# Optimization experiments

Measured on AMD Instinct MI355X. Metric: run time of the kernel, lower is better.

The kernel has to match this reference:

```python
import jax, jax.numpy as jnp
import numpy as np


def setup_inputs() -> dict:
    key = jax.random.key(0)
    ks = jax.random.split(key, 5)
    N, C, H, W = 4, 256, 64, 64
    fan_scale = 1.0 / np.sqrt(C)  # kaiming-ish scale for 1x1 conv weights
    x = jax.random.normal(ks[0], (N, C, H, W), dtype=jnp.float32)
    Wq = jax.random.normal(ks[1], (C, C), dtype=jnp.float32) * fan_scale
    Wk = jax.random.normal(ks[2], (C, C), dtype=jnp.float32) * fan_scale
    Wv = jax.random.normal(ks[3], (C, C), dtype=jnp.float32) * fan_scale
    bq = jnp.zeros((C,), dtype=jnp.float32)
    bk = jnp.zeros((C,), dtype=jnp.float32)
    bv = jnp.zeros((C,), dtype=jnp.float32)
    gamma = jax.random.uniform(ks[4], (1,), dtype=jnp.float32)
    return {"x": x, "Wq": Wq, "bq": bq, "Wk": Wk, "bk": bk, "Wv": Wv, "bv": bv, "gamma": gamma}


def reference(x, Wq, bq, Wk, bk, Wv, bv, gamma):
    # x: (N, C, H, W); 1x1 convs are channel-mixing matmuls.
    N, C, H, W = x.shape
    HW = H * W
    xf = x.reshape(N, C, HW)
    q = jnp.einsum('oc,ncl->nol', Wq, xf) + bq[None, :, None]  # (N, C, HW)
    k = jnp.einsum('oc,ncl->nol', Wk, xf) + bk[None, :, None]
    v = jnp.einsum('oc,ncl->nol', Wv, xf) + bv[None, :, None]
    # spatial mode: energy = softmax(Q^T K) over last dim (no 1/sqrt(d) scaling)
    energy = jax.nn.softmax(jnp.einsum('nci,ncj->nij', q, k), axis=-1)  # (N, HW, HW)
    # att[n,c,i] = sum_j v[n,c,j] * energy[n,i,j]  (bmm(value, energy^T))
    att = jnp.einsum('ncj,nij->nci', v, energy)  # (N, C, HW)
    # in_channels == out_channels -> residual is identity
    out = x + gamma[0] * att.reshape(N, C, H, W)
    return out
```

## Files before the change

### kernel.cpp

```cpp
#include <hip/hip_runtime.h>

typedef unsigned short ushort_t;
typedef unsigned int u32;
typedef _Float16 f16;
typedef f16 f16x8 __attribute__((ext_vector_type(8)));
typedef f16 f16x2 __attribute__((ext_vector_type(2)));
typedef ushort_t u16x8 __attribute__((ext_vector_type(8)));
typedef float f32x4 __attribute__((ext_vector_type(4)));
typedef float f32x16 __attribute__((ext_vector_type(16)));

#define C_DIM 256
#define HW 4096
#define CHW (C_DIM*HW)
#define L2E 1.4426950408889634f

__device__ __align__(16) f16 g_xbT[4 * CHW];
__device__ __align__(16) f16 g_q[4 * CHW];
__device__ __align__(16) f16 g_k[4 * CHW];
__device__ __align__(16) f16 g_v[4 * CHW];
__device__ __align__(16) f16 g_opart[16 * CHW];
__device__ __align__(16) float g_ml[16 * 2 * HW];
__device__ __align__(16) f16 g_wf[3 * 65536];
__device__ __align__(16) float g_bf[3 * 256];

__device__ __forceinline__ float bf2f(ushort_t h) {
    union { u32 u; float f; } v; v.u = ((u32)h) << 16; return v.f;
}
__device__ __forceinline__ ushort_t f2bf(float f) {
    union { float f; u32 u; } v; v.f = f;
    u32 r = v.u + 0x7FFF + ((v.u >> 16) & 1);
    return (ushort_t)(r >> 16);
}
__device__ __forceinline__ float fin0(float v) {
    return (v > -1e30f && v < 1e30f) ? v : 0.f;
}
__device__ __forceinline__ f16 sf16(float v) {
    return (f16)((v > -1e4f && v < 1e4f) ? v : 0.f);
}
__device__ __forceinline__ void gl2lds16(const f16* g, f16* l) {
    __builtin_amdgcn_global_load_lds(
        (const __attribute__((address_space(1))) u32*)g,
        (__attribute__((address_space(3))) u32*)l, 16, 0, 0);
}
__device__ __forceinline__ int probe_mode(const void* p) {
    int lane = threadIdx.x & 63;
    float v = fabsf(bf2f(((const ushort_t*)p)[lane]));
    v = (v < 1e6f) ? v : 1e6f;
#pragma unroll
    for (int d = 1; d < 64; d <<= 1) v += __shfl_xor(v, d, 64);
    return (v * (1.f / 64.f) > 100.f) ? 1 : 0;
}

__global__ void k_sentinel(ushort_t* out, int n) {
    int i = blockIdx.x * 256 + threadIdx.x;
    if (i < n) out[i] = f2bf(777.f);
}

__global__ __launch_bounds__(256) void k_wprep(
    const void* __restrict__ W0, const void* __restrict__ b0,
    const void* __restrict__ W1, const void* __restrict__ b1,
    const void* __restrict__ W2, const void* __restrict__ b2)
{
    int mat = blockIdx.y;
    const void* W = (mat == 0) ? W0 : (mat == 1) ? W1 : W2;
    const void* B = (mat == 0) ? b0 : (mat == 1) ? b1 : b2;
    int mode = probe_mode(W);
    int off = blockIdx.x * 2048 + threadIdx.x * 8;
    f16* dst = g_wf + mat * 65536 + off;
    f16x8 o;
    if (mode == 0) {
        u16x8 v = *(const u16x8*)((const ushort_t*)W + off);
#pragma unroll
        for (int e = 0; e < 8; ++e) o[e] = sf16(bf2f(v[e]));
    } else {
        const float* wf = (const float*)W + off;
        float4 a = *(const float4*)wf;
        float4 b = *(const float4*)(wf + 4);
        o[0]=sf16(a.x); o[1]=sf16(a.y); o[2]=sf16(a.z); o[3]=sf16(a.w);
        o[4]=sf16(b.x); o[5]=sf16(b.y); o[6]=sf16(b.z); o[7]=sf16(b.w);
    }
    *(f16x8*)dst = o;
    if (blockIdx.x == 0 && threadIdx.x < 32) {
#pragma unroll
        for (int e = 0; e < 8; ++e) {
            int i = threadIdx.x * 8 + e;
            g_bf[mat * 256 + i] = mode ? ((const float*)B)[i]
                                       : bf2f(((const ushort_t*)B)[i]);
        }
    }
}

__global__ __launch_bounds__(256) void k_transpose(const void* __restrict__ xv) {
    __shared__ f16 t[64][66];
    int mode = probe_mode(xv);
    int n = blockIdx.z, c0 = blockIdx.y * 64, l0 = blockIdx.x * 64;
    int tid = threadIdx.x;
    f16* ob = g_xbT + n * CHW;
    int lq = (tid & 15) * 4;
    int cl = tid >> 4;
    if (mode == 0) {
        const ushort_t* xb = (const ushort_t*)xv + n * CHW;
#pragma unroll
        for (int p = 0; p < 4; ++p) {
            int c = cl + 16 * p;
            ushort4 v = *(const ushort4*)(xb + (c0 + c) * HW + l0 + lq);
            t[lq + 0][c] = sf16(bf2f(v.x));
            t[lq + 1][c] = sf16(bf2f(v.y));
            t[lq + 2][c] = sf16(bf2f(v.z));
            t[lq + 3][c] = sf16(bf2f(v.w));
        }
    } else {
        const float* xb = (const float*)xv + n * CHW;
#pragma unroll
        for (int p = 0; p < 4; ++p) {
            int c = cl + 16 * p;
            float4 v = *(const float4*)(xb + (c0 + c) * HW + l0 + lq);
            t[lq + 0][c] = sf16(v.x);
            t[lq + 1][c] = sf16(v.y);
            t[lq + 2][c] = sf16(v.z);
            t[lq + 3][c] = sf16(v.w);
        }
    }
    __syncthreads();
    int c2 = (tid & 31) * 2;
    int lr = tid >> 5;
#pragma unroll
    for (int p = 0; p < 8; ++p) {
        int l = lr + 8 * p;
        u32 pair = *(const u32*)&t[l][c2];
        *(u32*)(ob + (l0 + l) * C_DIM + c0 + c2) = pair;
    }
}

__global__ __launch_bounds__(256) void k_proj() {
    __shared__ __align__(16) f16 lds_x[128 * 64];
    __shared__ __align__(16) f16 lds_w[128 * 64];
    int l0 = blockIdx.x * 128;
    int og0 = blockIdx.y * 128;
    int n = blockIdx.z;
    int mat = og0 >> 8;
    int om0 = og0 & 255;
    const f16* Wf = g_wf + mat * 65536;
    const float* Bf = g_bf + mat * 256;
    int tid = threadIdx.x, w = tid >> 6, lane = tid & 63;
    int quad = lane >> 4, l16 = lane & 15;
    const f16* xb = g_xbT + n * CHW;

    f32x4 acc[2][8];
#pragma unroll
    for (int a = 0; a < 2; a++)
#pragma unroll
        for (int b = 0; b < 8; b++) acc[a][b] = f32x4{0.f, 0.f, 0.f, 0.f};

    for (int ch = 0; ch < 4; ++ch) {
        int cc0 = ch * 64;
#pragma unroll
        for (int s = 0; s < 4; ++s) {
            int g = s * 256 + tid;
            int row = g >> 3, gp = (g & 7) ^ (row & 7);
            gl2lds16(xb + (l0 + row) * C_DIM + cc0 + gp * 8,
                     lds_x + (s * 256 + w * 64) * 8);
            gl2lds16(Wf + (om0 + row) * C_DIM + cc0 + gp * 8,
                     lds_w + (s * 256 + w * 64) * 8);
        }
        asm volatile("s_waitcnt vmcnt(0)" ::: "memory");
        __builtin_amdgcn_s_barrier();
        __builtin_amdgcn_sched_barrier(0);
#pragma unroll
        for (int ks = 0; ks < 2; ++ks) {
            f16x8 af[2];
#pragma unroll
            for (int mt = 0; mt < 2; ++mt) {
                int row = w * 32 + mt * 16 + l16;
                int g = ks * 4 + quad;
                int pos = g ^ (row & 7);
                af[mt] = *(const f16x8*)(lds_x + (row * 8 + pos) * 8);
            }
#pragma unroll
            for (int nt = 0; nt < 8; ++nt) {
                int rowo = nt * 16 + l16;
                int g = ks * 4 + quad;
                int pos = g ^ (rowo & 7);
                f16x8 bfv = *(const f16x8*)(lds_w + (rowo * 8 + pos) * 8);
                if (mat < 2) {
                    acc[0][nt] = __builtin_amdgcn_mfma_f32_16x16x32_f16(af[0], bfv, acc[0][nt], 0, 0, 0);
                    acc[1][nt] = __builtin_amdgcn_mfma_f32_16x16x32_f16(af[1], bfv, acc[1][nt], 0, 0, 0);
                } else {
                    acc[0][nt] = __builtin_amdgcn_mfma_f32_16x16x32_f16(bfv, af[0], acc[0][nt], 0, 0, 0);
                    acc[1][nt] = __builtin_amdgcn_mfma_f32_16x16x32_f16(bfv, af[1], acc[1][nt], 0, 0, 0);
                }
            }
        }
        __builtin_amdgcn_s_barrier();
    }

    if (mat < 2) {
        f16* T = ((mat == 0) ? g_q : g_k) + n * CHW;
        float bvv[8];
#pragma unroll
        for (int nt = 0; nt < 8; nt++) bvv[nt] = Bf[om0 + nt * 16 + l16];
#pragma unroll
        for (int mt = 0; mt < 2; mt++)
#pragma unroll
            for (int nt = 0; nt < 8; nt++)
#pragma unroll
                for (int r = 0; r < 4; r++) {
                    int l = l0 + w * 32 + mt * 16 + quad * 4 + r;
                    int o = om0 + nt * 16 + l16;
                    T[l * C_DIM + o] = sf16(acc[mt][nt][r] + bvv[nt]);
                }
    } else {
        f16* T = g_v + n * CHW;
#pragma unroll
        for (int mt = 0; mt < 2; mt++)
#pragma unroll
            for (int nt = 0; nt < 8; nt++)
#pragma unroll
                for (int r = 0; r < 4; r++) {
                    int o = om0 + nt * 16 + quad * 4 + r;
                    int l = l0 + w * 32 + mt * 16 + l16;
                    T[o * HW + l] = sf16(acc[mt][nt][r] + Bf[o]);
                }
    }
}

__device__ __forceinline__ f16x8 pack_pfrag(const float* p, int h) {
    union PK { u32 u; f16x2 h2; } t0, t1, t2, t3;
    t0.h2 = f16x2{(f16)p[0], (f16)p[1]};
    t1.h2 = f16x2{(f16)p[2], (f16)p[3]};
    t2.h2 = f16x2{(f16)p[4], (f16)p[5]};
    t3.h2 = f16x2{(f16)p[6], (f16)p[7]};
    u32 sa = __shfl_xor(t0.u, 32, 64);
    u32 sb = __shfl_xor(t1.u, 32, 64);
    u32 sc = __shfl_xor(t2.u, 32, 64);
    u32 sd = __shfl_xor(t3.u, 32, 64);
    union RW { u32 w[4]; f16x8 v; } r;
    r.w[0] = h ? sc : t0.u;
    r.w[1] = h ? sd : t1.u;
    r.w[2] = h ? t2.u : sa;
    r.w[3] = h ? t3.u : sb;
    return r.v;
}

__global__ __launch_bounds__(256, 2) void k_attn() {
    __shared__ __align__(16) f16 smem[32768];
    f16* kbuf = smem;
    f16* vbuf = smem + 16384;

    int bid = blockIdx.x;
    int x8 = bid & 7;
    int n = x8 >> 1, jhi = x8 & 1;
    int rest = bid >> 3;
    int jlo = rest & 1;
    int i0 = (rest >> 1) * 128;
    int jq = jhi * 2 + jlo;
    int tid = threadIdx.x, w = tid >> 6, lane = tid & 63;
    int j5 = lane & 31, h = lane >> 5;

    const f16* Qb = g_q + n * CHW;
    const f16* Kb = g_k + n * CHW;
    const f16* Vb = g_v + n * CHW;

    f16x8 qf[16];
    {
        const f16* qrow = Qb + (i0 + w * 32 + j5) * C_DIM + h * 8;
#pragma unroll
        for (int ck = 0; ck < 16; ++ck)
            qf[ck] = *(const f16x8*)(qrow + ck * 16);
    }

    int k_lane = h * 256 + j5 * 8;
    int v_lane = h * 2048 + j5 * 8;

    const f16* ksrc = Kb + (jq * 1024 + j5) * C_DIM + (w * 2 + h) * 8;
    const f16* vsrc = Vb + tid * HW + jq * 1024;
    int dst_w = w * 512;

    f32x16 o_acc[8];
#pragma unroll
    for (int ct = 0; ct < 8; ++ct)
#pragma unroll
        for (int r = 0; r < 16; ++r) o_acc[ct][r] = 0.f;

    float m_ = -1e30f, l_ = 0.f, al_prev = 1.f;
    f16x8 pf0 = {}, pf1 = {};

#pragma unroll
    for (int s = 0; s < 4; ++s) gl2lds16(ksrc + s * 64, kbuf + s * 2048 + dst_w);
    ksrc += 32 * C_DIM;
    asm volatile("s_waitcnt vmcnt(0)" ::: "memory");
    __builtin_amdgcn_s_barrier();
    __builtin_amdgcn_sched_barrier(0);

    for (int it = 0; it < 31; ++it) {
        int kcur = it & 1;
#pragma unroll
        for (int s = 0; s < 4; ++s)
            gl2lds16(ksrc + s * 64, kbuf + (kcur ^ 1) * 8192 + s * 2048 + dst_w);
        ksrc += 32 * C_DIM;
        __builtin_amdgcn_sched_barrier(0);
#pragma unroll
        for (int s = 0; s < 4; ++s)
            gl2lds16(vsrc + s * 8, vbuf + kcur * 8192 + s * 2048 + dst_w);
        vsrc += 32;
        __builtin_amdgcn_sched_barrier(0);

        const f16* kb = kbuf + kcur * 8192 + k_lane;
        f32x16 sa, sb;
#pragma unroll
        for (int r = 0; r < 16; ++r) { sa[r] = 0.f; sb[r] = 0.f; }
        __builtin_amdgcn_s_setprio(1);
#pragma unroll
        for (int ck = 0; ck < 16; ++ck) {
            f16x8 kf = *(const f16x8*)(kb + ck * 512);
            if (ck & 1) sb = __builtin_amdgcn_mfma_f32_32x32x16_f16(kf, qf[ck], sb, 0, 0, 0);
            else        sa = __builtin_amdgcn_mfma_f32_32x32x16_f16(kf, qf[ck], sa, 0, 0, 0);
        }
        __builtin_amdgcn_s_setprio(0);
        f32x16 st;
#pragma unroll
        for (int r = 0; r < 16; ++r) st[r] = sa[r] + sb[r];

        asm volatile("s_waitcnt vmcnt(8)" ::: "memory");
        __builtin_amdgcn_s_barrier();
        __builtin_amdgcn_sched_barrier(0);

        if (it > 0) {
            if (__any(al_prev < 1.f)) {
#pragma unroll
                for (int ct = 0; ct < 8; ++ct)
#pragma unroll
                    for (int r = 0; r < 16; ++r) o_acc[ct][r] *= al_prev;
            }
            const f16* vb = vbuf + (kcur ^ 1) * 8192 + v_lane;
            __builtin_amdgcn_s_setprio(1);
#pragma unroll
            for (int ct = 0; ct < 8; ++ct) {
                f16x8 v0 = *(const f16x8*)(vb + ct * 256);
                f16x8 v1 = *(const f16x8*)(vb + 4096 + ct * 256);
                o_acc[ct] = __builtin_amdgcn_mfma_f32_32x32x16_f16(v0, pf0, o_acc[ct], 0, 0, 0);
                o_acc[ct] = __builtin_amdgcn_mfma_f32_32x32x16_f16(v1, pf1, o_acc[ct], 0, 0, 0);
            }
            __builtin_amdgcn_s_setprio(0);
        }

        float mx0 = fmaxf(fmaxf(st[0], st[1]), fmaxf(st[2], st[3]));
        float mx1 = fmaxf(fmaxf(st[4], st[5]), fmaxf(st[6], st[7]));
        float mx2 = fmaxf(fmaxf(st[8], st[9]), fmaxf(st[10], st[11]));
        float mx3 = fmaxf(fmaxf(st[12], st[13]), fmaxf(st[14], st[15]));
        float smax = fmaxf(fmaxf(mx0, mx1), fmaxf(mx2, mx3));
        smax = fmaxf(smax, __shfl_xor(smax, 32, 64));
        float mq = __builtin_ceilf(smax * 0.125f) * 8.f;
        float mn = fmaxf(m_, mq);
        float al = __builtin_amdgcn_exp2f((m_ - mn) * L2E);
        float nl = -mn * L2E;
        float p[16];
#pragma unroll
        for (int r = 0; r < 16; ++r)
            p[r] = __builtin_amdgcn_exp2f(st[r] * L2E + nl);
        float a0 = (p[0] + p[1]) + (p[2] + p[3]);
        float a1 = (p[4] + p[5]) + (p[6] + p[7]);
        float a2 = (p[8] + p[9]) + (p[10] + p[11]);
        float a3 = (p[12] + p[13]) + (p[14] + p[15]);
        float rs = (a0 + a1) + (a2 + a3);
        m_ = mn;
        l_ = l_ * al + rs;
        al_prev = al;
        pf0 = pack_pfrag(p, h);
        pf1 = pack_pfrag(p + 8, h);

        asm volatile("s_waitcnt vmcnt(4)" ::: "memory");
        __builtin_amdgcn_s_barrier();
        __builtin_amdgcn_sched_barrier(0);
    }

    {
#pragma unroll
        for (int s = 0; s < 4; ++s)
            gl2lds16(vsrc + s * 8, vbuf + 8192 + s * 2048 + dst_w);
        __builtin_amdgcn_sched_barrier(0);

        const f16* kb = kbuf + 8192 + k_lane;
        f32x16 sa, sb;
#pragma unroll
        for (int r = 0; r < 16; ++r) { sa[r] = 0.f; sb[r] = 0.f; }
        __builtin_amdgcn_s_setprio(1);
#pragma unroll
        for (int ck = 0; ck < 16; ++ck) {
            f16x8 kf = *(const f16x8*)(kb + ck * 512);
            if (ck & 1) sb = __builtin_amdgcn_mfma_f32_32x32x16_f16(kf, qf[ck], sb, 0, 0, 0);
            else        sa = __builtin_amdgcn_mfma_f32_32x32x16_f16(kf, qf[ck], sa, 0, 0, 0);
        }
        __builtin_amdgcn_s_setprio(0);
        f32x16 st;
#pragma unroll
        for (int r = 0; r < 16; ++r) st[r] = sa[r] + sb[r];

        asm volatile("s_waitcnt vmcnt(4)" ::: "memory");
        __builtin_amdgcn_s_barrier();
        __builtin_amdgcn_sched_barrier(0);

        if (__any(al_prev < 1.f)) {
#pragma unroll
            for (int ct = 0; ct < 8; ++ct)
#pragma unroll
                for (int r = 0; r < 16; ++r) o_acc[ct][r] *= al_prev;
        }
        {
            const f16* vb = vbuf + v_lane;
            __builtin_amdgcn_s_setprio(1);
#pragma unroll
            for (int ct = 0; ct < 8; ++ct) {
                f16x8 v0 = *(const f16x8*)(vb + ct * 256);
                f16x8 v1 = *(const f16x8*)(vb + 4096 + ct * 256);
                o_acc[ct] = __builtin_amdgcn_mfma_f32_32x32x16_f16(v0, pf0, o_acc[ct], 0, 0, 0);
                o_acc[ct] = __builtin_amdgcn_mfma_f32_32x32x16_f16(v1, pf1, o_acc[ct], 0, 0, 0);
            }
            __builtin_amdgcn_s_setprio(0);
        }
        float mx0 = fmaxf(fmaxf(st[0], st[1]), fmaxf(st[2], st[3]));
        float mx1 = fmaxf(fmaxf(st[4], st[5]), fmaxf(st[6], st[7]));
        float mx2 = fmaxf(fmaxf(st[8], st[9]), fmaxf(st[10], st[11]));
        float mx3 = fmaxf(fmaxf(st[12], st[13]), fmaxf(st[14], st[15]));
        float smax = fmaxf(fmaxf(mx0, mx1), fmaxf(mx2, mx3));
        smax = fmaxf(smax, __shfl_xor(smax, 32, 64));
        float mq = __builtin_ceilf(smax * 0.125f) * 8.f;
        float mn = fmaxf(m_, mq);
        float al = __builtin_amdgcn_exp2f((m_ - mn) * L2E);
        float nl = -mn * L2E;
        float p[16];
#pragma unroll
        for (int r = 0; r < 16; ++r)
            p[r] = __builtin_amdgcn_exp2f(st[r] * L2E + nl);
        float a0 = (p[0] + p[1]) + (p[2] + p[3]);
        float a1 = (p[4] + p[5]) + (p[6] + p[7]);
        float a2 = (p[8] + p[9]) + (p[10] + p[11]);
        float a3 = (p[12] + p[13]) + (p[14] + p[15]);
        float rs = (a0 + a1) + (a2 + a3);
        m_ = mn;
        l_ = l_ * al + rs;
        al_prev = al;
        pf0 = pack_pfrag(p, h);
        pf1 = pack_pfrag(p + 8, h);

        asm volatile("s_waitcnt vmcnt(0)" ::: "memory");
        __builtin_amdgcn_s_barrier();
        __builtin_amdgcn_sched_barrier(0);

        if (__any(al_prev < 1.f)) {
#pragma unroll
            for (int ct = 0; ct < 8; ++ct)
#pragma unroll
                for (int r = 0; r < 16; ++r) o_acc[ct][r] *= al_prev;
        }
        const f16* vb = vbuf + 8192 + v_lane;
#pragma unroll
        for (int ct = 0; ct < 8; ++ct) {
            f16x8 v0 = *(const f16x8*)(vb + ct * 256);
            f16x8 v1 = *(const f16x8*)(vb + 4096 + ct * 256);
            o_acc[ct] = __builtin_amdgcn_mfma_f32_32x32x16_f16(v0, pf0, o_acc[ct], 0, 0, 0);
            o_acc[ct] = __builtin_amdgcn_mfma_f32_32x32x16_f16(v1, pf1, o_acc[ct], 0, 0, 0);
        }
    }

    l_ += __shfl_xor(l_, 32, 64);

    int slot = jq * 4 + n;
    int i_out = i0 + w * 32 + j5;
    if (h == 0) {
        g_ml[(slot * 2 + 0) * HW + i_out] = m_;
        g_ml[(slot * 2 + 1) * HW + i_out] = l_;
    }
    float inv = (l_ > 1e-30f) ? 1.f / l_ : 0.f;
    f16* ob = g_opart + slot * CHW + i_out;
#pragma unroll
    for (int ct = 0; ct < 8; ++ct) {
        int cbase = ct * 32 + 4 * h;
#pragma unroll
        for (int r = 0; r < 16; ++r) {
            int c = cbase + (r & 3) + 8 * (r >> 2);
            ob[c * HW] = (f16)(o_acc[ct][r] * inv);
        }
    }
}

__global__ __launch_bounds__(256) void k_combine(
    const void* __restrict__ xv, const void* __restrict__ gv, void* __restrict__ outv)
{
    int mode = probe_mode(xv);
    float gam = fin0(mode ? ((const float*)gv)[0] : bf2f(((const ushort_t*)gv)[0]));
    int n = blockIdx.y;
    int off = blockIdx.x * 2048 + threadIdx.x * 8;
    int i = off & (HW - 1);

    u16x8 op[4];
    float ms[4][8], ls[4][8];
#pragma unroll
    for (int s = 0; s < 4; ++s) {
        int slot = s * 4 + n;
        op[s] = *(const u16x8*)((const ushort_t*)g_opart + slot * CHW + off);
        float4 mA = *(const float4*)&g_ml[(slot * 2 + 0) * HW + i];
        float4 mB = *(const float4*)&g_ml[(slot * 2 + 0) * HW + i + 4];
        float4 lA = *(const float4*)&g_ml[(slot * 2 + 1) * HW + i];
        float4 lB = *(const float4*)&g_ml[(slot * 2 + 1) * HW + i + 4];
        ms[s][0]=mA.x; ms[s][1]=mA.y; ms[s][2]=mA.z; ms[s][3]=mA.w;
        ms[s][4]=mB.x; ms[s][5]=mB.y; ms[s][6]=mB.z; ms[s][7]=mB.w;
        ls[s][0]=lA.x; ls[s][1]=lA.y; ls[s][2]=lA.z; ls[s][3]=lA.w;
        ls[s][4]=lB.x; ls[s][5]=lB.y; ls[s][6]=lB.z; ls[s][7]=lB.w;
    }

    float o[8];
#pragma unroll
    for (int e = 0; e < 8; ++e) {
        float m = fmaxf(fmaxf(ms[0][e], ms[1][e]), fmaxf(ms[2][e], ms[3][e]));
        float num = 0.f, den = 0.f;
#pragma unroll
        for (int s = 0; s < 4; ++s) {
            float wgt = __builtin_amdgcn_exp2f((ms[s][e] - m) * L2E) * ls[s][e];
            union { ushort_t u; f16 h; } cv; cv.u = (ushort_t)op[s][e];
            num += wgt * (float)cv.h;
            den += wgt;
        }
        o[e] = (den > 1e-30f) ? num / den : 0.f;
    }

    if (mode == 0) {
        u16x8 xp = *(const u16x8*)((const ushort_t*)xv + n * CHW + off);
        u16x8 res;
#pragma unroll
        for (int e = 0; e < 8; ++e)
            res[e] = f2bf(fin0(bf2f((ushort_t)xp[e]) + gam * o[e]));
        *(u16x8*)((ushort_t*)outv + n * CHW + off) = res;
    } else {
        const float* xb = (const float*)xv + n * CHW + off;
        float* outb = (float*)outv + n * CHW + off;
        float4 xA = *(const float4*)xb;
        float4 xB = *(const float4*)(xb + 4);
        float4 rA, rB;
        rA.x = fin0(xA.x + gam * o[0]); rA.y = fin0(xA.y + gam * o[1]);
        rA.z = fin0(xA.z + gam * o[2]); rA.w = fin0(xA.w + gam * o[3]);
        rB.x = fin0(xB.x + gam * o[4]); rB.y = fin0(xB.y + gam * o[5]);
        rB.z = fin0(xB.z + gam * o[6]); rB.w = fin0(xB.w + gam * o[7]);
        *(float4*)outb = rA;
        *(float4*)(outb + 4) = rB;
    }
}

extern "C" void kernel_launch(void* const* d_in, const int* in_sizes, int n_in,
                              void* d_out, int out_size, void* d_ws, size_t ws_size,
                              hipStream_t stream) {
    (void)d_ws; (void)ws_size;
    bool ok = (n_in == 8) &&
              in_sizes[0] == 4 * CHW &&
              in_sizes[1] == C_DIM * C_DIM && in_sizes[2] == C_DIM &&
              in_sizes[3] == C_DIM * C_DIM && in_sizes[4] == C_DIM &&
              in_sizes[5] == C_DIM * C_DIM && in_sizes[6] == C_DIM &&
              in_sizes[7] == 1 && out_size == 4 * CHW;
    if (!ok) {
        hipLaunchKernelGGL(k_sentinel, dim3((out_size + 255) / 256), dim3(256), 0, stream,
                           (ushort_t*)d_out, out_size);
        return;
    }
    hipLaunchKernelGGL(k_wprep, dim3(32, 3), dim3(256), 0, stream,
                       d_in[1], d_in[2], d_in[3], d_in[4], d_in[5], d_in[6]);
    hipLaunchKernelGGL(k_transpose, dim3(64, 4, 4), dim3(256), 0, stream, d_in[0]);
    hipLaunchKernelGGL(k_proj, dim3(32, 6, 4), dim3(256), 0, stream);
    hipLaunchKernelGGL(k_attn, dim3(512), dim3(256), 0, stream);
    hipLaunchKernelGGL(k_combine, dim3(CHW / 2048, 4), dim3(256), 0, stream,
                       d_in[0], d_in[7], d_out);
}
```

Measured before the change: 219.9 us.

## Merge weight prep into transpose kernel and double-buffer projection weight tiles

The weight/bias conversion kernel and the input transpose kernel are merged into one launch, with an extra grid z-slice handling the weights. This removes one kernel launch and lets the two independent jobs run together. In the projection GEMM, the weight tile gets a second LDS buffer and the next chunk is prefetched while MFMAs run on the current one. The x tile is still single-buffered and reloaded after a barrier, so only part of the load latency is hidden, at the cost of more LDS per block and extra barriers.

Result: faster. 212.7 us (-3.2%).

```diff
diff --git a/kernel.cpp b/kernel.cpp
--- a/kernel.cpp
+++ b/kernel.cpp
@@ -56,41 +56,43 @@
     if (i < n) out[i] = f2bf(777.f);
 }
 
-__global__ __launch_bounds__(256) void k_wprep(
+__global__ __launch_bounds__(256) void k_prep(
+    const void* __restrict__ xv,
     const void* __restrict__ W0, const void* __restrict__ b0,
     const void* __restrict__ W1, const void* __restrict__ b1,
     const void* __restrict__ W2, const void* __restrict__ b2)
 {
-    int mat = blockIdx.y;
-    const void* W = (mat == 0) ? W0 : (mat == 1) ? W1 : W2;
-    const void* B = (mat == 0) ? b0 : (mat == 1) ? b1 : b2;
-    int mode = probe_mode(W);
-    int off = blockIdx.x * 2048 + threadIdx.x * 8;
-    f16* dst = g_wf + mat * 65536 + off;
-    f16x8 o;
-    if (mode == 0) {
-        u16x8 v = *(const u16x8*)((const ushort_t*)W + off);
-#pragma unroll
-        for (int e = 0; e < 8; ++e) o[e] = sf16(bf2f(v[e]));
-    } else {
-        const float* wf = (const float*)W + off;
-        float4 a = *(const float4*)wf;
-        float4 b = *(const float4*)(wf + 4);
-        o[0]=sf16(a.x); o[1]=sf16(a.y); o[2]=sf16(a.z); o[3]=sf16(a.w);
-        o[4]=sf16(b.x); o[5]=sf16(b.y); o[6]=sf16(b.z); o[7]=sf16(b.w);
-    }
-    *(f16x8*)dst = o;
-    if (blockIdx.x == 0 && threadIdx.x < 32) {
-#pragma unroll
-        for (int e = 0; e < 8; ++e) {
-            int i = threadIdx.x * 8 + e;
-            g_bf[mat * 256 + i] = mode ? ((const float*)B)[i]
-                                       : bf2f(((const ushort_t*)B)[i]);
-        }
-    }
-}
-
-__global__ __launch_bounds__(256) void k_transpose(const void* __restrict__ xv) {
+    if (blockIdx.z == 4) {
+        int mat = blockIdx.y;
+        if (mat >= 3 || blockIdx.x >= 32) return;
+        const void* W = (mat == 0) ? W0 : (mat == 1) ? W1 : W2;
+        const void* B = (mat == 0) ? b0 : (mat == 1) ? b1 : b2;
+        int mode = probe_mode(W);
+        int off = blockIdx.x * 2048 + threadIdx.x * 8;
+        f16* dst = g_wf + mat * 65536 + off;
+        f16x8 o;
+        if (mode == 0) {
+            u16x8 v = *(const u16x8*)((const ushort_t*)W + off);
+#pragma unroll
+            for (int e = 0; e < 8; ++e) o[e] = sf16(bf2f(v[e]));
+        } else {
+            const float* wf = (const float*)W + off;
+            float4 a = *(const float4*)wf;
+            float4 b = *(const float4*)(wf + 4);
+            o[0]=sf16(a.x); o[1]=sf16(a.y); o[2]=sf16(a.z); o[3]=sf16(a.w);
+            o[4]=sf16(b.x); o[5]=sf16(b.y); o[6]=sf16(b.z); o[7]=sf16(b.w);
+        }
+        *(f16x8*)dst = o;
+        if (blockIdx.x == 0 && threadIdx.x < 32) {
+#pragma unroll
+            for (int e = 0; e < 8; ++e) {
+                int i = threadIdx.x * 8 + e;
+                g_bf[mat * 256 + i] = mode ? ((const float*)B)[i]
+                                           : bf2f(((const ushort_t*)B)[i]);
+            }
+        }
+        return;
+    }
     __shared__ f16 t[64][66];
     int mode = probe_mode(xv);
     int n = blockIdx.z, c0 = blockIdx.y * 64, l0 = blockIdx.x * 64;
@@ -134,7 +136,7 @@
 
 __global__ __launch_bounds__(256) void k_proj() {
     __shared__ __align__(16) f16 lds_x[128 * 64];
-    __shared__ __align__(16) f16 lds_w[128 * 64];
+    __shared__ __align__(16) f16 lds_w[2][128 * 64];
     int l0 = blockIdx.x * 128;
     int og0 = blockIdx.y * 128;
     int n = blockIdx.z;
@@ -146,25 +148,40 @@
     int quad = lane >> 4, l16 = lane & 15;
     const f16* xb = g_xbT + n * CHW;
 
+    int srow[4], sgp[4];
+#pragma unroll
+    for (int s = 0; s < 4; ++s) {
+        int g = s * 256 + tid;
+        srow[s] = g >> 3;
+        sgp[s] = (g & 7) ^ (srow[s] & 7);
+    }
+
     f32x4 acc[2][8];
 #pragma unroll
     for (int a = 0; a < 2; a++)
 #pragma unroll
         for (int b = 0; b < 8; b++) acc[a][b] = f32x4{0.f, 0.f, 0.f, 0.f};
+
+#pragma unroll
+    for (int s = 0; s < 4; ++s) {
+        gl2lds16(xb + (l0 + srow[s]) * C_DIM + 0 + sgp[s] * 8,
+                 lds_x + (s * 256 + w * 64) * 8);
+        gl2lds16(Wf + (om0 + srow[s]) * C_DIM + 0 + sgp[s] * 8,
+                 lds_w[0] + (s * 256 + w * 64) * 8);
+    }
+    asm volatile("s_waitcnt vmcnt(0)" ::: "memory");
+    __builtin_amdgcn_s_barrier();
+    __builtin_amdgcn_sched_barrier(0);
 
     for (int ch = 0; ch < 4; ++ch) {
         int cc0 = ch * 64;
-#pragma unroll
-        for (int s = 0; s < 4; ++s) {
-            int g = s * 256 + tid;
-            int row = g >> 3, gp = (g & 7) ^ (row & 7);
-            gl2lds16(xb + (l0 + row) * C_DIM + cc0 + gp * 8,
-                     lds_x + (s * 256 + w * 64) * 8);
-            gl2lds16(Wf + (om0 + row) * C_DIM + cc0 + gp * 8,
-                     lds_w + (s * 256 + w * 64) * 8);
-        }
-        asm volatile("s_waitcnt vmcnt(0)" ::: "memory");
-        __builtin_amdgcn_s_barrier();
+        int cur = ch & 1;
+        if (ch < 3) {
+#pragma unroll
+            for (int s = 0; s < 4; ++s)
+                gl2lds16(Wf + (om0 + srow[s]) * C_DIM + (cc0 + 64) + sgp[s] * 8,
+                         lds_w[cur ^ 1] + (s * 256 + w * 64) * 8);
+        }
         __builtin_amdgcn_sched_barrier(0);
 #pragma unroll
         for (int ks = 0; ks < 2; ++ks) {
@@ -181,7 +198,7 @@
                 int rowo = nt * 16 + l16;
                 int g = ks * 4 + quad;
                 int pos = g ^ (rowo & 7);
-                f16x8 bfv = *(const f16x8*)(lds_w + (rowo * 8 + pos) * 8);
+                f16x8 bfv = *(const f16x8*)(lds_w[cur] + (rowo * 8 + pos) * 8);
                 if (mat < 2) {
                     acc[0][nt] = __builtin_amdgcn_mfma_f32_16x16x32_f16(af[0], bfv, acc[0][nt], 0, 0, 0);
                     acc[1][nt] = __builtin_amdgcn_mfma_f32_16x16x32_f16(af[1], bfv, acc[1][nt], 0, 0, 0);
@@ -192,6 +209,16 @@
             }
         }
         __builtin_amdgcn_s_barrier();
+        __builtin_amdgcn_sched_barrier(0);
+        if (ch < 3) {
+#pragma unroll
+            for (int s = 0; s < 4; ++s)
+                gl2lds16(xb + (l0 + srow[s]) * C_DIM + (cc0 + 64) + sgp[s] * 8,
+                         lds_x + (s * 256 + w * 64) * 8);
+            asm volatile("s_waitcnt vmcnt(0)" ::: "memory");
+            __builtin_amdgcn_s_barrier();
+            __builtin_amdgcn_sched_barrier(0);
+        }
     }
 
     if (mat < 2) {
@@ -561,9 +588,8 @@
                            (ushort_t*)d_out, out_size);
         return;
     }
-    hipLaunchKernelGGL(k_wprep, dim3(32, 3), dim3(256), 0, stream,
-                       d_in[1], d_in[2], d_in[3], d_in[4], d_in[5], d_in[6]);
-    hipLaunchKernelGGL(k_transpose, dim3(64, 4, 4), dim3(256), 0, stream, d_in[0]);
+    hipLaunchKernelGGL(k_prep, dim3(64, 4, 5), dim3(256), 0, stream,
+                       d_in[0], d_in[1], d_in[2], d_in[3], d_in[4], d_in[5], d_in[6]);
     hipLaunchKernelGGL(k_proj, dim3(32, 6, 4), dim3(256), 0, stream);
     hipLaunchKernelGGL(k_attn, dim3(512), dim3(256), 0, stream);
     hipLaunchKernelGGL(k_combine, dim3(CHW / 2048, 4), dim3(256), 0, stream,
```
